# Kernel tuning notes

Measured on AMD Instinct MI355X. Metric: run time of the kernel, lower is better.

The kernel has to match this reference:

```python
import jax, jax.numpy as jnp
import numpy as np

V, H, I, L = 32000, 1024, 2048, 4
NH, NKV, HD = 16, 8, 64
E, K = 4, 2
B, S = 2, 1024
NEG = jnp.finfo(jnp.float32).min


def setup_inputs() -> dict:
    key = jax.random.key(0)
    ks = jax.random.split(key, 11)
    w = lambda k, shape: jax.random.normal(k, shape, jnp.float32) * 0.02
    return dict(
        input_ids=jax.random.randint(ks[0], (B, S), 0, V),
        embed=w(ks[1], (V, H)),
        Wq=w(ks[2], (L, H, NH * HD)),
        Wk=w(ks[3], (L, H, NKV * HD)),
        Wv=w(ks[4], (L, H, NKV * HD)),
        Wo=w(ks[5], (L, NH * HD, H)),
        ln1=jnp.ones((L, H), jnp.float32),
        ln2=jnp.ones((L, H), jnp.float32),
        gate=w(ks[6], (L, H, E)),
        Wg=w(ks[7], (L, E, H, I)),
        Wu=w(ks[8], (L, E, H, I)),
        Wd=w(ks[9], (L, E, I, H)),
        norm_w=jnp.ones((H,), jnp.float32),
        lm_head=w(ks[10], (H, V)),
    )


def rmsnorm(x, w, eps=1e-6):
    var = jnp.mean(x * x, axis=-1, keepdims=True)
    return w * (x * jax.lax.rsqrt(var + eps))


def forward(input_ids, embed, Wq, Wk, Wv, Wo, ln1, ln2, gate, Wg, Wu, Wd, norm_w, lm_head):
    b, s = input_ids.shape
    h = embed[input_ids]  # [B,S,H]
    mask = jnp.where(jnp.triu(jnp.ones((s, s), bool), 1), NEG, 0.0)[None, None]  # causal [1,1,S,S]
    inv_sqrt_hd = 1.0 / np.sqrt(HD)
    rep = NH // NKV

    def step(h, p):
        wq, wk, wv, wo, l1, l2, gw, wg, wu, wd = p
        x = rmsnorm(h, l1)
        q = (x @ wq).reshape(b, s, NH, HD).transpose(0, 2, 1, 3)    # [B,NH,S,HD]
        k = (x @ wk).reshape(b, s, NKV, HD).transpose(0, 2, 1, 3)   # [B,NKV,S,HD]
        v = (x @ wv).reshape(b, s, NKV, HD).transpose(0, 2, 1, 3)
        k = jnp.repeat(k, rep, axis=1)  # GQA repeat_kv
        v = jnp.repeat(v, rep, axis=1)
        scores = jnp.einsum('bhqd,bhkd->bhqk', q, k) * inv_sqrt_hd + mask
        attn = jax.nn.softmax(scores, axis=-1)
        o = jnp.einsum('bhqk,bhkd->bhqd', attn, v).transpose(0, 2, 1, 3).reshape(b, s, NH * HD)
        h = h + o @ wo
        # MoE FFN (top-k routing, combine via per-expert gate weights)
        x = rmsnorm(h, l2).reshape(b * s, H)              # [T,H]
        probs = jax.nn.softmax(x @ gw, axis=-1)           # [T,E]
        topk_p, topk_i = jax.lax.top_k(probs, K)          # [T,K]
        comb = jnp.sum(topk_p[..., None] * jax.nn.one_hot(topk_i, E, dtype=x.dtype), axis=1)  # [T,E]
        g = jax.nn.silu(jnp.einsum('th,ehi->eti', x, wg))  # [E,T,I]
        u = jnp.einsum('th,ehi->eti', x, wu)
        eo = jnp.einsum('eti,eih->eth', g * u, wd)         # [E,T,H]
        moe = jnp.einsum('eth,te->th', eo, comb).reshape(b, s, H)
        return h + moe, None

    h, _ = jax.lax.scan(step, h, (Wq, Wk, Wv, Wo, ln1, ln2, gate, Wg, Wu, Wd))
    return rmsnorm(h, norm_w) @ lm_head  # [B,S,V]


def reference(input_ids, embed, Wq, Wk, Wv, Wo, ln1, ln2, gate, Wg, Wu, Wd, norm_w, lm_head):
    return forward(input_ids, embed, Wq, Wk, Wv, Wo, ln1, ln2, gate, Wg, Wu, Wd, norm_w, lm_head)
```

## Files before the change

kernel.cpp:

```cpp
#include <hip/hip_runtime.h>

#define T_ 2048
#define H_ 1024
#define S_ 1024
#define V_ 32000
#define I_ 2048
#define NHD 1024
#define KVD 512

typedef unsigned short u16;
typedef unsigned int u32;
typedef __attribute__((ext_vector_type(8))) short s16x8;
typedef __attribute__((ext_vector_type(4))) float f32x4;

__device__ __forceinline__ u16 f2b(float f){ u32 x=__builtin_bit_cast(u32,f); return (u16)((x+0x7fffu+((x>>16)&1u))>>16); }
__device__ __forceinline__ float b2f(u16 u){ return __builtin_bit_cast(float,(u32)u<<16); }
__device__ __forceinline__ float wsum(float v){ for(int o=32;o;o>>=1) v+=__shfl_xor(v,o); return v; }
__device__ __forceinline__ float wmax(float v){ for(int o=32;o;o>>=1) v=fmaxf(v,__shfl_xor(v,o)); return v; }

__device__ __forceinline__ void gl16(const void* g, void* l){
  __builtin_amdgcn_global_load_lds(
      (const __attribute__((address_space(1))) unsigned int*)g,
      (__attribute__((address_space(3))) unsigned int*)l, 16, 0, 0);
}

__global__ void k_embed(const int* __restrict__ ids, const float* __restrict__ emb, float* __restrict__ h){
  int t = blockIdx.x;
  long src = (long)ids[t]*H_;
  ((float4*)(h + (long)t*H_))[threadIdx.x] = ((const float4*)(emb+src))[threadIdx.x];
}

__global__ void k_zero(int* c){ if(threadIdx.x<16) c[threadIdx.x]=0; }

__global__ void k_rms_sp(const float* __restrict__ h, const float* __restrict__ w,
                         u16* __restrict__ xhi, u16* __restrict__ xlo){
  int wid = threadIdx.x>>6, lane = threadIdx.x&63;
  int t = blockIdx.x*4 + wid;
  const float* row = h + (long)t*H_;
  float v[16]; float ss=0.f;
  #pragma unroll
  for(int j=0;j<16;j++){ v[j]=row[j*64+lane]; ss += v[j]*v[j]; }
  ss = wsum(ss);
  float rstd = rsqrtf(ss/(float)H_ + 1e-6f);
  #pragma unroll
  for(int j=0;j<16;j++){
    int idx=j*64+lane;
    float y = v[j]*rstd*w[idx];
    u16 hv = f2b(y);
    xhi[(long)t*H_+idx] = hv;
    xlo[(long)t*H_+idx] = f2b(y - b2f(hv));
  }
}

__global__ void k_router(const float* __restrict__ h, const float* __restrict__ lw,
                         const float* __restrict__ gate, float* __restrict__ comb,
                         int* __restrict__ lists, int* __restrict__ cnt, int2* __restrict__ epos,
                         u16* __restrict__ xhi, u16* __restrict__ xlo){
  int wid = threadIdx.x>>6, lane = threadIdx.x&63;
  int t = blockIdx.x*4+wid;
  const float* row = h + (long)t*H_;
  float v[16]; float ss=0.f;
  #pragma unroll
  for(int j=0;j<16;j++){ v[j]=row[j*64+lane]; ss+=v[j]*v[j]; }
  ss = wsum(ss);
  float rstd = rsqrtf(ss/(float)H_+1e-6f);
  float a0=0,a1=0,a2=0,a3=0;
  #pragma unroll
  for(int j=0;j<16;j++){
    int idx=j*64+lane;
    float y = v[j]*rstd*lw[idx];
    u16 hv = f2b(y);
    xhi[(long)t*H_+idx] = hv;
    xlo[(long)t*H_+idx] = f2b(y - b2f(hv));
    float4 g4 = ((const float4*)gate)[idx];
    a0 += y*g4.x; a1 += y*g4.y; a2 += y*g4.z; a3 += y*g4.w;
  }
  a0=wsum(a0); a1=wsum(a1); a2=wsum(a2); a3=wsum(a3);
  if(lane==0){
    float p[4]={a0,a1,a2,a3};
    float m = fmaxf(fmaxf(p[0],p[1]),fmaxf(p[2],p[3]));
    float s=0; for(int e=0;e<4;e++){ p[e]=__expf(p[e]-m); s+=p[e]; }
    for(int e=0;e<4;e++) p[e]/=s;
    int i1=0; for(int e=1;e<4;e++) if(p[e]>p[i1]) i1=e;
    int i2=-1; for(int e=0;e<4;e++){ if(e==i1) continue; if(i2<0||p[e]>p[i2]) i2=e; }
    float* c = comb + (long)t*4;
    for(int e=0;e<4;e++) c[e] = (e==i1||e==i2)? p[e] : 0.f;
    int p1 = atomicAdd(&cnt[i1],1); lists[i1*T_+p1]=t;
    int p2 = atomicAdd(&cnt[i2],1); lists[i2*T_+p2]=t;
    epos[t] = make_int2((p1<<2)|i1, (p2<<2)|i2);
  }
}

__global__ void k_transpose(const float* __restrict__ in, u16* __restrict__ hi, u16* __restrict__ lo,
                            int R, int C, long zi, long zo){
  __shared__ float tile[32][33];
  in += (long)blockIdx.z*zi; hi += (long)blockIdx.z*zo; if(lo) lo += (long)blockIdx.z*zo;
  int c0 = blockIdx.x*32, r0 = blockIdx.y*32;
  int tx = threadIdx.x, ty = threadIdx.y;
  #pragma unroll
  for(int i=0;i<4;i++) tile[ty+8*i][tx] = in[(long)(r0+ty+8*i)*C + c0+tx];
  __syncthreads();
  #pragma unroll
  for(int i=0;i<4;i++){
    int cc=ty+8*i; float v = tile[tx][cc];
    u16 hv = f2b(v);
    long idx = (long)(c0+cc)*R + r0+tx;
    hi[idx] = hv;
    if(lo) lo[idx] = f2b(v - b2f(hv));
  }
}

__global__ void k_wtrans(const float* __restrict__ Wq, const float* __restrict__ Wk,
                         const float* __restrict__ Wv, const float* __restrict__ Wo,
                         const float* __restrict__ Wg, const float* __restrict__ Wu,
                         const float* __restrict__ Wd,
                         u16* __restrict__ qkvh, u16* __restrict__ qkvl,
                         u16* __restrict__ oh, u16* __restrict__ ol,
                         u16* __restrict__ gh, u16* __restrict__ gl_,
                         u16* __restrict__ uh, u16* __restrict__ ul,
                         u16* __restrict__ dh, u16* __restrict__ dl)
{
  __shared__ float tile[32][33];
  int id = blockIdx.x;
  const float* in; u16 *hi, *lo; int R, C, bx, by;
  if(id < 1024){ in=Wq; hi=qkvh; lo=qkvl; R=1024; C=1024; bx=id&31; by=id>>5; }
  else if(id < 1536){ id-=1024; in=Wk; hi=qkvh+1048576; lo=qkvl+1048576; R=1024; C=512; bx=id&15; by=id>>4; }
  else if(id < 2048){ id-=1536; in=Wv; hi=qkvh+1572864; lo=qkvl+1572864; R=1024; C=512; bx=id&15; by=id>>4; }
  else if(id < 3072){ id-=2048; in=Wo; hi=oh; lo=ol; R=1024; C=1024; bx=id&31; by=id>>5; }
  else if(id < 11264){ id-=3072; int z=id>>11, r2=id&2047;
    in=Wg+(size_t)z*H_*I_; hi=gh+(size_t)z*I_*H_; lo=gl_+(size_t)z*I_*H_;
    R=1024; C=2048; bx=r2&63; by=r2>>6; }
  else if(id < 19456){ id-=11264; int z=id>>11, r2=id&2047;
    in=Wu+(size_t)z*H_*I_; hi=uh+(size_t)z*I_*H_; lo=ul+(size_t)z*I_*H_;
    R=1024; C=2048; bx=r2&63; by=r2>>6; }
  else { id-=19456; int z=id>>11, r2=id&2047;
    in=Wd+(size_t)z*I_*H_; hi=dh+(size_t)z*H_*I_; lo=dl+(size_t)z*H_*I_;
    R=2048; C=1024; bx=r2&31; by=r2>>5; }
  int c0=bx*32, r0=by*32, tx=threadIdx.x, ty=threadIdx.y;
  #pragma unroll
  for(int i=0;i<4;i++) tile[ty+8*i][tx] = in[(long)(r0+ty+8*i)*C + c0+tx];
  __syncthreads();
  #pragma unroll
  for(int i=0;i<4;i++){
    int cc=ty+8*i; float v = tile[tx][cc];
    u16 hv = f2b(v);
    long idx = (long)(c0+cc)*R + r0+tx;
    hi[idx] = hv;
    lo[idx] = f2b(v - b2f(hv));
  }
}

__global__ void k_combine(float* __restrict__ h, const float* __restrict__ eo,
                          const int2* __restrict__ epos, const float* __restrict__ comb){
  int t = blockIdx.x, c = threadIdx.x;
  int2 ep = epos[t];
  int e1 = ep.x&3, p1 = ep.x>>2, e2 = ep.y&3, p2 = ep.y>>2;
  float c1 = comb[t*4+e1], c2 = comb[t*4+e2];
  float4 a = ((const float4*)(eo + (long)(e1*T_+p1)*H_))[c];
  float4 b = ((const float4*)(eo + (long)(e2*T_+p2)*H_))[c];
  float4* hp = (float4*)(h + (long)t*H_) + c;
  float4 hv = *hp;
  hv.x += c1*a.x + c2*b.x; hv.y += c1*a.y + c2*b.y;
  hv.z += c1*a.z + c2*b.z; hv.w += c1*a.w + c2*b.w;
  *hp = hv;
}

__global__ __launch_bounds__(256) void k_flash(
  const u16* __restrict__ qh_g, const u16* __restrict__ ql_g,
  const u16* __restrict__ kh_g, const u16* __restrict__ kl_g,
  const u16* __restrict__ vth_g, const u16* __restrict__ vtl_g,
  u16* __restrict__ oh_g, u16* __restrict__ ol_g)
{
  __shared__ alignas(16) u16 Qh[4096], Ql[4096];
  __shared__ alignas(16) u16 KVh[8192], KVl[8192];
  __shared__ alignas(16) u16 Ph[8192], Pl[8192];
  const int qt = blockIdx.x, hh = blockIdx.y, b = blockIdx.z;
  const int hk = hh>>1;
  const int lane = threadIdx.x&63, w = threadIdx.x>>6;
  const int rA = lane&15, kg = (lane>>4)*8;

  {
    const u16* qp = qh_g + ((long)(b*1024+qt*64))*NHD + hh*64;
    const u16* qp2= ql_g + ((long)(b*1024+qt*64))*NHD + hh*64;
    #pragma unroll
    for(int s=0;s<2;s++){
      int idx=s*4+w, hf=idx>>2, g=idx&3;
      int row = g*16 + (lane>>2);
      int c8  = hf*32 + (lane&3)*8;
      gl16(qp  + (long)row*NHD + c8, &Qh[hf*2048 + g*512]);
      gl16(qp2 + (long)row*NHD + c8, &Ql[hf*2048 + g*512]);
    }
  }

  f32x4 Oa[4];
  float mrun[4], lrun[4];
  #pragma unroll
  for(int jn=0;jn<4;jn++){ f32x4 zv={0.f,0.f,0.f,0.f}; Oa[jn]=zv; }
  #pragma unroll
  for(int r=0;r<4;r++){ mrun[r]=-3.0e38f; lrun[r]=0.f; }

  const int ktend = (qt>>1)+1;
  for(int kt=0; kt<ktend; kt++){
    __syncthreads();
    {
      const u16* kp = kh_g + ((long)(b*1024+kt*128))*KVD + hk*64;
      const u16* kp2= kl_g + ((long)(b*1024+kt*128))*KVD + hk*64;
      #pragma unroll
      for(int s=0;s<4;s++){
        int idx=s*4+w, hf=idx>>3, g=idx&7;
        int row = g*16 + (lane>>2);
        int c8  = hf*32 + (lane&3)*8;
        gl16(kp  + (long)row*KVD + c8, &KVh[hf*4096 + g*512]);
        gl16(kp2 + (long)row*KVD + c8, &KVl[hf*4096 + g*512]);
      }
    }
    __syncthreads();

    f32x4 Sf[8];
    #pragma unroll
    for(int j=0;j<8;j++){ f32x4 zv={0.f,0.f,0.f,0.f}; Sf[j]=zv; }
    #pragma unroll
    for(int k2=0;k2<2;k2++){
      s16x8 ah,al,bh[8],bl[8];
      int q = w*16+rA;
      ah=*(const s16x8*)&Qh[k2*2048 + q*32 + kg];
      al=*(const s16x8*)&Ql[k2*2048 + q*32 + kg];
      #pragma unroll
      for(int j=0;j<8;j++){
        int ky = j*16+rA;
        bh[j]=*(const s16x8*)&KVh[k2*4096 + ky*32 + kg];
        bl[j]=*(const s16x8*)&KVl[k2*4096 + ky*32 + kg];
      }
      #pragma unroll
      for(int j=0;j<8;j++){
        Sf[j]=__builtin_amdgcn_mfma_f32_16x16x32_bf16(ah,bh[j],Sf[j],0,0,0);
        Sf[j]=__builtin_amdgcn_mfma_f32_16x16x32_bf16(ah,bl[j],Sf[j],0,0,0);
        Sf[j]=__builtin_amdgcn_mfma_f32_16x16x32_bf16(al,bh[j],Sf[j],0,0,0);
      }
    }

    const bool last = (kt==ktend-1);
    #pragma unroll
    for(int j=0;j<8;j++)
      #pragma unroll
      for(int r=0;r<4;r++){
        float sv = Sf[j][r]*0.125f;
        if(last){
          int qr = qt*64 + w*16 + ((lane>>4)<<2) + r;
          int ky = kt*128 + j*16 + (lane&15);
          if(ky>qr) sv = -3.0e38f;
        }
        Sf[j][r]=sv;
      }

    float mt[4];
    #pragma unroll
    for(int r=0;r<4;r++){
      float v = Sf[0][r];
      #pragma unroll
      for(int j=1;j<8;j++) v = fmaxf(v, Sf[j][r]);
      v=fmaxf(v,__shfl_xor(v,1)); v=fmaxf(v,__shfl_xor(v,2));
      v=fmaxf(v,__shfl_xor(v,4)); v=fmaxf(v,__shfl_xor(v,8));
      mt[r]=v;
    }

    #pragma unroll
    for(int r=0;r<4;r++){
      float mo=mrun[r];
      float mn=fmaxf(mo,mt[r]);
      float al_=__expf(mo-mn);
      mrun[r]=mn;
      lrun[r]*=al_;
      #pragma unroll
      for(int jn=0;jn<4;jn++) Oa[jn][r]*=al_;
    }

    float ls[4];
    #pragma unroll
    for(int r=0;r<4;r++) ls[r]=0.f;
    #pragma unroll
    for(int j=0;j<8;j++)
      #pragma unroll
      for(int r=0;r<4;r++){
        int q  = w*16+((lane>>4)<<2)+r;
        int ky = j*16+(lane&15);
        float pv=__expf(Sf[j][r]-mrun[r]);
        ls[r]+=pv;
        u16 hv=f2b(pv);
        int a=(ky>>5)*2048 + q*32 + (ky&31);
        Ph[a]=hv; Pl[a]=f2b(pv-b2f(hv));
      }
    #pragma unroll
    for(int r=0;r<4;r++){
      float v=ls[r];
      v+=__shfl_xor(v,1); v+=__shfl_xor(v,2); v+=__shfl_xor(v,4); v+=__shfl_xor(v,8);
      lrun[r]+=v;
    }
    __syncthreads();

    {
      const u16* vp = vth_g + (long)b*((long)KVD*S_) + (long)(hk*64)*S_ + kt*128;
      const u16* vp2= vtl_g + (long)b*((long)KVD*S_) + (long)(hk*64)*S_ + kt*128;
      #pragma unroll
      for(int s=0;s<4;s++){
        int idx=s*4+w, ks=idx>>2, g=idx&3;
        int dr = g*16 + (lane>>2);
        int k8 = (lane&3)*8;
        gl16(vp  + (long)dr*S_ + ks*32 + k8, &KVh[ks*2048 + g*512]);
        gl16(vp2 + (long)dr*S_ + ks*32 + k8, &KVl[ks*2048 + g*512]);
      }
    }
    __syncthreads();

    #pragma unroll
    for(int ks=0;ks<4;ks++){
      s16x8 pah,pal,vbh[4],vbl[4];
      int q = w*16+rA;
      pah=*(const s16x8*)&Ph[ks*2048 + q*32 + kg];
      pal=*(const s16x8*)&Pl[ks*2048 + q*32 + kg];
      #pragma unroll
      for(int jn=0;jn<4;jn++){
        int d = jn*16+rA;
        vbh[jn]=*(const s16x8*)&KVh[ks*2048 + d*32 + kg];
        vbl[jn]=*(const s16x8*)&KVl[ks*2048 + d*32 + kg];
      }
      #pragma unroll
      for(int jn=0;jn<4;jn++){
        Oa[jn]=__builtin_amdgcn_mfma_f32_16x16x32_bf16(pah,vbh[jn],Oa[jn],0,0,0);
        Oa[jn]=__builtin_amdgcn_mfma_f32_16x16x32_bf16(pah,vbl[jn],Oa[jn],0,0,0);
        Oa[jn]=__builtin_amdgcn_mfma_f32_16x16x32_bf16(pal,vbh[jn],Oa[jn],0,0,0);
      }
    }
  }

  #pragma unroll
  for(int jn=0;jn<4;jn++)
    #pragma unroll
    for(int r=0;r<4;r++){
      long t = (long)b*1024 + qt*64 + w*16+((lane>>4)<<2)+r;
      int col = hh*64 + jn*16 + (lane&15);
      float ov = Oa[jn][r] / lrun[r];
      u16 hv=f2b(ov);
      oh_g[t*NHD+col]=hv;
      ol_g[t*NHD+col]=f2b(ov-b2f(hv));
    }
}

__global__ __launch_bounds__(256) void k_qkv(
  const u16* __restrict__ xhi, const u16* __restrict__ xlo,
  const u16* __restrict__ Bh, const u16* __restrict__ Bl,
  u16* __restrict__ qhi, u16* __restrict__ qlo,
  u16* __restrict__ khi, u16* __restrict__ klo,
  u16* __restrict__ vthi, u16* __restrict__ vtlo)
{
  __shared__ alignas(16) u16 As[2*128*64], Bs[2*128*64];
  const int m0=blockIdx.x*128, n0=blockIdx.y*128;
  const int tid=threadIdx.x, lane=tid&63, w=tid>>6, wr=w>>1, wc=w&1;
  const int rsub = lane>>3;
  const int col8 = ((lane&7) ^ (rsub&7))*8;
  const int kq = lane>>4;
  f32x4 acc[4][4];
  #pragma unroll
  for(int i=0;i<4;i++)
    #pragma unroll
    for(int j=0;j<4;j++){ f32x4 zv={0.f,0.f,0.f,0.f}; acc[i][j]=zv; }

  for(int kt=0;kt<16;kt++){
    const int k0=kt*64;
    __syncthreads();
    #pragma unroll
    for(int s=0;s<4;s++){
      int ch=s*4+w; int row=ch*8+rsub;
      gl16(xhi + (long)(m0+row)*H_ + k0+col8, &As[ch*512]);
      gl16(xlo + (long)(m0+row)*H_ + k0+col8, &As[8192+ch*512]);
      gl16(Bh  + (long)(n0+row)*H_ + k0+col8, &Bs[ch*512]);
      gl16(Bl  + (long)(n0+row)*H_ + k0+col8, &Bs[8192+ch*512]);
    }
    __syncthreads();
    #pragma unroll
    for(int ks=0;ks<2;ks++){
      s16x8 ah[4],al[4],bh[4],bl[4];
      #pragma unroll
      for(int i=0;i<4;i++){
        int row = wr*64+i*16+(lane&15);
        int sl = ((ks*4+kq) ^ (row&7))*8;
        ah[i]=*(const s16x8*)&As[row*64+sl];
        al[i]=*(const s16x8*)&As[8192+row*64+sl];
      }
      #pragma unroll
      for(int j=0;j<4;j++){
        int row = wc*64+j*16+(lane&15);
        int sl = ((ks*4+kq) ^ (row&7))*8;
        bh[j]=*(const s16x8*)&Bs[row*64+sl];
        bl[j]=*(const s16x8*)&Bs[8192+row*64+sl];
      }
      #pragma unroll
      for(int i=0;i<4;i++)
        #pragma unroll
        for(int j=0;j<4;j++){
          acc[i][j]=__builtin_amdgcn_mfma_f32_16x16x32_bf16(ah[i],bh[j],acc[i][j],0,0,0);
          acc[i][j]=__builtin_amdgcn_mfma_f32_16x16x32_bf16(ah[i],bl[j],acc[i][j],0,0,0);
          acc[i][j]=__builtin_amdgcn_mfma_f32_16x16x32_bf16(al[i],bh[j],acc[i][j],0,0,0);
        }
    }
  }

  #pragma unroll
  for(int i=0;i<4;i++){
    #pragma unroll
    for(int j=0;j<4;j++){
      const int gm0 = m0 + wr*64 + i*16 + ((lane>>4)<<2);
      const int gn  = n0 + wc*64 + j*16 + (lane&15);
      #pragma unroll
      for(int r=0;r<4;r++){
        const int gm = gm0+r;
        float v = acc[i][j][r];
        u16 hv = f2b(v);
        u16 lv = f2b(v - b2f(hv));
        if(gn < 1024){
          long idx=(long)gm*NHD+gn; qhi[idx]=hv; qlo[idx]=lv;
        } else if(gn < 1536){
          long idx=(long)gm*KVD+(gn-1024); khi[idx]=hv; klo[idx]=lv;
        } else {
          long idx=((long)(gm>>10)<<19) + (long)(gn-1536)*S_ + (gm&1023);
          vthi[idx]=hv; vtlo[idx]=lv;
        }
      }
    }
  }
}

__global__ __launch_bounds__(256) void k_moe_ug(
  const u16* __restrict__ xhi, const u16* __restrict__ xlo,
  const u16* __restrict__ Wuh, const u16* __restrict__ Wul,
  const u16* __restrict__ Wgh, const u16* __restrict__ Wgl,
  u16* __restrict__ guh, u16* __restrict__ gul,
  const int* __restrict__ lists, const int* __restrict__ cntp)
{
  const int bb = blockIdx.x;
  const int xcd = bb&7, bidx = bb>>3;
  const int grp = xcd + 8*(bidx>>4);
  const int mslot = bidx&15;
  const int e = grp>>5;
  const int n0 = (grp&31)*64;
  const int m0 = mslot*128;
  const int ce = cntp[e];
  if(m0>=ce) return;
  const int* ridx = lists + e*T_;
  const u16* Buh_g = Wuh + (size_t)e*H_*I_;
  const u16* Bul_g = Wul + (size_t)e*H_*I_;
  const u16* Bgh_g = Wgh + (size_t)e*H_*I_;
  const u16* Bgl_g = Wgl + (size_t)e*H_*I_;
  __shared__ alignas(16) u16 Ah[128*64], Al[128*64];
  __shared__ alignas(16) u16 Buh[64*64], Bul[64*64], Bgh[64*64], Bgl[64*64];
  const int tid=threadIdx.x, lane=tid&63, w=tid>>6;
  const int wr=w>>1, wc=w&1;
  const int rsub = lane>>3;
  const int col8 = ((lane&7) ^ (rsub&7))*8;
  const int kq = lane>>4;
  int arA[4];
  #pragma unroll
  for(int s=0;s<4;s++){ int idx=m0 + (s*4+w)*8 + rsub; arA[s]=ridx[idx<ce?idx:ce-1]; }
  f32x4 au[4][2], ag[4][2];
  #pragma unroll
  for(int i=0;i<4;i++)
    #pragma unroll
    for(int j=0;j<2;j++){ f32x4 zv={0.f,0.f,0.f,0.f}; au[i][j]=zv; ag[i][j]=zv; }

  for(int kt=0;kt<16;kt++){
    const int k0=kt*64;
    __syncthreads();
    #pragma unroll
    for(int s=0;s<4;s++){
      int ch=s*4+w;
      gl16(xhi + (long)arA[s]*H_ + k0+col8, &Ah[ch*512]);
      gl16(xlo + (long)arA[s]*H_ + k0+col8, &Al[ch*512]);
    }
    #pragma unroll
    for(int s=0;s<2;s++){
      int ch=s*4+w;
      int brow = n0 + ch*8 + rsub;
      gl16(Buh_g + (long)brow*H_ + k0+col8, &Buh[ch*512]);
      gl16(Bul_g + (long)brow*H_ + k0+col8, &Bul[ch*512]);
      gl16(Bgh_g + (long)brow*H_ + k0+col8, &Bgh[ch*512]);
      gl16(Bgl_g + (long)brow*H_ + k0+col8, &Bgl[ch*512]);
    }
    __syncthreads();
    #pragma unroll
    for(int ks=0;ks<2;ks++){
      s16x8 fah[4],fal[4],fbuh[2],fbul[2],fbgh[2],fbgl[2];
      #pragma unroll
      for(int i=0;i<4;i++){
        int row = wr*64+i*16+(lane&15);
        int sl = ((ks*4+kq) ^ (row&7))*8;
        fah[i]=*(const s16x8*)&Ah[row*64+sl];
        fal[i]=*(const s16x8*)&Al[row*64+sl];
      }
      #pragma unroll
      for(int j=0;j<2;j++){
        int row = wc*32+j*16+(lane&15);
        int sl = ((ks*4+kq) ^ (row&7))*8;
        fbuh[j]=*(const s16x8*)&Buh[row*64+sl];
        fbul[j]=*(const s16x8*)&Bul[row*64+sl];
        fbgh[j]=*(const s16x8*)&Bgh[row*64+sl];
        fbgl[j]=*(const s16x8*)&Bgl[row*64+sl];
      }
      #pragma unroll
      for(int i=0;i<4;i++)
        #pragma unroll
        for(int j=0;j<2;j++){
          au[i][j]=__builtin_amdgcn_mfma_f32_16x16x32_bf16(fah[i],fbuh[j],au[i][j],0,0,0);
          au[i][j]=__builtin_amdgcn_mfma_f32_16x16x32_bf16(fah[i],fbul[j],au[i][j],0,0,0);
          au[i][j]=__builtin_amdgcn_mfma_f32_16x16x32_bf16(fal[i],fbuh[j],au[i][j],0,0,0);
          ag[i][j]=__builtin_amdgcn_mfma_f32_16x16x32_bf16(fah[i],fbgh[j],ag[i][j],0,0,0);
          ag[i][j]=__builtin_amdgcn_mfma_f32_16x16x32_bf16(fah[i],fbgl[j],ag[i][j],0,0,0);
          ag[i][j]=__builtin_amdgcn_mfma_f32_16x16x32_bf16(fal[i],fbgh[j],ag[i][j],0,0,0);
        }
    }
  }

  #pragma unroll
  for(int i=0;i<4;i++){
    #pragma unroll
    for(int j=0;j<2;j++){
      const int gm0 = m0 + wr*64 + i*16 + ((lane>>4)<<2);
      const int gn  = n0 + wc*32 + j*16 + (lane&15);
      #pragma unroll
      for(int r=0;r<4;r++){
        const int gm = gm0+r;
        if(gm<ce){
          float uu=au[i][j][r], gg=ag[i][j][r];
          float val = (gg/(1.f+__expf(-gg)))*uu;
          long idx = (long)(e*T_+gm)*I_ + gn;
          u16 hv=f2b(val);
          guh[idx]=hv; gul[idx]=f2b(val-b2f(hv));
        }
      }
    }
  }
}

template<int BM,int BN,int WM,int WN,int BKT,bool SPL,int EPI,int CM,int GATH,bool SWZ>
__launch_bounds__(WM*WN*64)
__global__ void k_gemm(const u16* __restrict__ Ahip, const u16* __restrict__ Alop,
                       const u16* __restrict__ Bhip, const u16* __restrict__ Blop,
                       void* __restrict__ Cp, void* __restrict__ auxp,
                       const int* __restrict__ cntp,
                       int Kdim, int lda, int ldb, int ldc,
                       long zA, long zB, int zBdiv, long zC,
                       float scale)
{
  constexpr int NT = WM*WN*64;
  constexpr int Wv = NT/64;
  constexpr int WMT = BM/WM, WNT = BN/WN;
  constexpr int MF = WMT/16, NF = WNT/16;
  constexpr int LPR = BKT/8;
  constexpr int LR  = 64/LPR;
  constexpr int ACn = (BM/LR)/Wv;
  constexpr int BCn = (BN/LR)/Wv;
  constexpr int KS  = BKT/32;
  static_assert(ACn>=1 && BCn>=1, "chunks");
  __shared__ alignas(16) u16 As[(SPL?2:1)*BM*BKT];
  __shared__ alignas(16) u16 Bs[(SPL?2:1)*BN*BKT];
  __shared__ float Cs[EPI==8?WM:1][EPI==8?16:1][EPI==8?(BN+4):1];
  constexpr int SL = T_/BM;
  int m0, n0, eid_ = 0, cnt = 0;
  if constexpr (GATH==3){
    eid_ = blockIdx.x/SL; m0 = (blockIdx.x%SL)*BM;
    cnt = cntp[eid_]; if(m0>=cnt) return;
    n0 = blockIdx.y*BN;
  } else if constexpr (GATH==4){
    constexpr int NTN = H_/BN;
    const int bb = blockIdx.x;
    const int xcd = bb&7, bidx = bb>>3;
    const int grp = xcd + 8*(bidx/SL);
    const int mslot = bidx%SL;
    eid_ = grp/NTN; n0 = (grp%NTN)*BN; m0 = mslot*BM;
    cnt = cntp[eid_]; if(m0>=cnt) return;
  } else if constexpr (SWZ){
    int nx = gridDim.x;
    int l = blockIdx.y*nx + blockIdx.x;
    int q = (nx*gridDim.y)>>3;
    int wid = (l&7)*q + (l>>3);
    m0 = (wid % nx)*BM; n0 = (wid / nx)*BN;
  } else {
    m0 = blockIdx.x*BM; n0 = blockIdx.y*BN;
  }
  if (CM==1 && n0 > m0) return;
  const int z = blockIdx.z;
  const int tid = threadIdx.x, lane = tid&63, w = tid>>6;
  const int wr = w/WN, wc = w%WN;
  const int rsub = lane/LPR;
  const int col8 = (((lane%LPR) ^ (rsub&(LPR-1))))*8;
  const int kq = lane>>4;
  const u16* Ahi = Ahip + (long)z*zA + (GATH>=3 ? (long)eid_*T_*lda : 0);
  const u16* Alo = SPL ? (Alop + (long)z*zA + (GATH>=3 ? (long)eid_*T_*lda : 0)) : (const u16*)nullptr;
  const u16* Bh  = Bhip + (long)(z/zBdiv)*zB + (GATH>=3 ? (long)eid_*zB : 0);
  const u16* Bl  = SPL ? (Blop + (long)(z/zBdiv)*zB + (GATH>=3 ? (long)eid_*zB : 0)) : (const u16*)nullptr;

  f32x4 acc[MF][NF];
  #pragma unroll
  for(int i=0;i<MF;i++)
    #pragma unroll
    for(int j=0;j<NF;j++){ f32x4 zv={0.f,0.f,0.f,0.f}; acc[i][j]=zv; }

  int ktend = Kdim/BKT;
  if (CM==2){ int lim=(m0+BM)/BKT; if(lim<ktend) ktend=lim; }

  for(int kt=0;kt<ktend;kt++){
    const int k0 = kt*BKT;
    __syncthreads();
    #pragma unroll
    for(int s=0;s<ACn;s++){
      int ch = s*Wv + w;
      int arow = m0 + ch*LR + rsub;
      if constexpr (GATH>=3){ arow = arow < cnt ? arow : cnt-1; }
      gl16(Ahi + (long)arow*lda + k0+col8, &As[ch*512]);
      if constexpr (SPL) gl16(Alo + (long)arow*lda + k0+col8, &As[BM*BKT + ch*512]);
    }
    #pragma unroll
    for(int s=0;s<BCn;s++){
      int ch = s*Wv + w;
      int brow = n0 + ch*LR + rsub;
      gl16(Bh + (long)brow*ldb + k0+col8, &Bs[ch*512]);
      if constexpr (SPL) gl16(Bl + (long)brow*ldb + k0+col8, &Bs[BN*BKT + ch*512]);
    }
    __syncthreads();
    #pragma unroll
    for(int ks=0;ks<KS;ks++){
      s16x8 ah[MF], al[MF], bh[NF], bl[NF];
      #pragma unroll
      for(int i=0;i<MF;i++){
        int row = wr*WMT+i*16+(lane&15);
        int sl = ((ks*4+kq) ^ (row&(LPR-1)))*8;
        ah[i]=*(const s16x8*)&As[row*BKT+sl];
        if constexpr (SPL) al[i]=*(const s16x8*)&As[BM*BKT+row*BKT+sl];
      }
      #pragma unroll
      for(int j=0;j<NF;j++){
        int row = wc*WNT+j*16+(lane&15);
        int sl = ((ks*4+kq) ^ (row&(LPR-1)))*8;
        bh[j]=*(const s16x8*)&Bs[row*BKT+sl];
        if constexpr (SPL) bl[j]=*(const s16x8*)&Bs[BN*BKT+row*BKT+sl];
      }
      #pragma unroll
      for(int i=0;i<MF;i++)
        #pragma unroll
        for(int j=0;j<NF;j++){
          acc[i][j]=__builtin_amdgcn_mfma_f32_16x16x32_bf16(ah[i],bh[j],acc[i][j],0,0,0);
          if constexpr (SPL){
            acc[i][j]=__builtin_amdgcn_mfma_f32_16x16x32_bf16(ah[i],bl[j],acc[i][j],0,0,0);
            acc[i][j]=__builtin_amdgcn_mfma_f32_16x16x32_bf16(al[i],bh[j],acc[i][j],0,0,0);
          }
        }
    }
  }

  if constexpr (EPI==8){
    float* C = (float*)Cp + (long)z*zC;
    #pragma unroll
    for(int i=0;i<MF;i++){
      __syncthreads();
      #pragma unroll
      for(int j=0;j<NF;j++)
        #pragma unroll
        for(int r=0;r<4;r++)
          Cs[wr][((lane>>4)<<2)+r][wc*WNT + j*16 + (lane&15)] = acc[i][j][r]*scale;
      __syncthreads();
      const int rrow = tid>>3;
      const int wri = rrow>>4, r16 = rrow&15;
      const long gm = m0 + wri*WMT + i*16 + r16;
      #pragma unroll
      for(int s=0;s<BN/32;s++){
        int c0 = ((tid&7) + s*8)*4;
        float4 vv = { Cs[wri][r16][c0], Cs[wri][r16][c0+1], Cs[wri][r16][c0+2], Cs[wri][r16][c0+3] };
        *(float4*)(C + gm*ldc + n0 + c0) = vv;
      }
    }
    return;
  }

  #pragma unroll
  for(int i=0;i<MF;i++){
    #pragma unroll
    for(int j=0;j<NF;j++){
      const int gm0 = m0 + wr*WMT + i*16 + ((lane>>4)<<2);
      const int gn  = n0 + wc*WNT + j*16 + (lane&15);
      #pragma unroll
      for(int r=0;r<4;r++){
        const int gm = gm0+r;
        const float v = acc[i][j][r];
        const bool live = (GATH==0) || (gm < cnt);
        if constexpr (EPI==1){
          if(live) ((float*)Cp + (long)z*zC)[(long)gm*ldc+gn] = v*scale;
        } else if constexpr (EPI==2){
          float* C = (float*)Cp; C[(long)gm*ldc+gn] += v;
        } else if constexpr (EPI==7){
          if(live) ((float*)Cp)[(long)(eid_*T_+gm)*ldc+gn] = v*scale;
        } else if constexpr (EPI==9){
          u16* Ch = (u16*)Cp + (long)z*zC;
          u16* Cl = (u16*)auxp + (long)z*zC;
          long idx = (long)gm*ldc+gn;
          u16 hv = f2b(v);
          Ch[idx]=hv; Cl[idx]=f2b(v-b2f(hv));
        }
      }
    }
  }
}

extern "C" void kernel_launch(void* const* d_in, const int* in_sizes, int n_in,
                              void* d_out, int out_size, void* d_ws, size_t ws_size,
                              hipStream_t stream)
{
  (void)in_sizes; (void)n_in; (void)out_size;
  const int*   ids   = (const int*)d_in[0];
  const float* emb   = (const float*)d_in[1];
  const float* Wq    = (const float*)d_in[2];
  const float* Wk    = (const float*)d_in[3];
  const float* Wv    = (const float*)d_in[4];
  const float* Wo    = (const float*)d_in[5];
  const float* ln1   = (const float*)d_in[6];
  const float* ln2   = (const float*)d_in[7];
  const float* gate  = (const float*)d_in[8];
  const float* Wg    = (const float*)d_in[9];
  const float* Wu    = (const float*)d_in[10];
  const float* Wd    = (const float*)d_in[11];
  const float* normw = (const float*)d_in[12];
  const float* lmh   = (const float*)d_in[13];

  char* p = (char*)d_ws;
  auto carve = [&](size_t bytes)->void*{ void* r=p; p += (bytes+255)&~(size_t)255; return r; };
  float* h    = (float*)carve((size_t)T_*H_*4);
  u16*   xhi  = (u16*)  carve((size_t)T_*H_*2);
  u16*   xlo  = (u16*)  carve((size_t)T_*H_*2);
  u16*   qhi  = (u16*)  carve((size_t)T_*NHD*2);
  u16*   qlo  = (u16*)  carve((size_t)T_*NHD*2);
  u16*   khi  = (u16*)  carve((size_t)T_*KVD*2);
  u16*   klo  = (u16*)  carve((size_t)T_*KVD*2);
  u16*   vthi = (u16*)  carve((size_t)T_*KVD*2);
  u16*   vtlo = (u16*)  carve((size_t)T_*KVD*2);
  u16*   ohi  = (u16*)  carve((size_t)T_*NHD*2);
  u16*   olo  = (u16*)  carve((size_t)T_*NHD*2);
  float* comb = (float*)carve((size_t)T_*4*4);
  int*   cnt  = (int*)  carve((size_t)16*4);
  int*   lists= (int*)  carve((size_t)4*T_*4);
  int2*  epos = (int2*) carve((size_t)T_*8);
  char*  U    = (char*) carve((size_t)112*1024*1024);
  u16*   wp   = (u16*)  carve((size_t)56623104*2);
  if ((size_t)(p - (char*)d_ws) > ws_size) return;

  u16*   guh  = (u16*)U;
  u16*   gul  = (u16*)(U + 33554432);
  float* eo   = (float*)(U + 67108864);

  u16 *WqkvTh = wp,          *WqkvTl = wp+2097152;
  u16 *WoTh = wp+4194304,    *WoTl = wp+5242880;
  u16 *WgTh = wp+6291456,    *WgTl = wp+14680064;
  u16 *WuTh = wp+23068672,   *WuTl = wp+31457280;
  u16 *WdTh = wp+39845888,   *WdTl = wp+48234496;

  dim3 tb(32,8);

  k_embed<<<T_,256,0,stream>>>(ids, emb, h);
  k_zero<<<1,64,0,stream>>>(cnt);

  for(int l=0;l<4;l++){
    k_wtrans<<<27648,tb,0,stream>>>(
      Wq+(size_t)l*H_*NHD, Wk+(size_t)l*H_*KVD, Wv+(size_t)l*H_*KVD, Wo+(size_t)l*NHD*H_,
      Wg+(size_t)l*4*H_*I_, Wu+(size_t)l*4*H_*I_, Wd+(size_t)l*4*I_*H_,
      WqkvTh, WqkvTl, WoTh, WoTl, WgTh, WgTl, WuTh, WuTl, WdTh, WdTl);

    k_rms_sp<<<T_/4,256,0,stream>>>(h, ln1+(size_t)l*H_, xhi, xlo);

    k_qkv<<<dim3(16,16),256,0,stream>>>(xhi, xlo, WqkvTh, WqkvTl, qhi, qlo, khi, klo, vthi, vtlo);

    k_flash<<<dim3(16,16,2),256,0,stream>>>(qhi, qlo, khi, klo, vthi, vtlo, ohi, olo);

    k_gemm<64,128,2,2,64,true,2,0,0,false><<<dim3(32,8,1),256,0,stream>>>(
      ohi, olo, WoTh, WoTl, h, nullptr, nullptr, NHD, NHD, NHD, H_, 0,0,1,0, 0.f);

    k_router<<<T_/4,256,0,stream>>>(h, ln2+(size_t)l*H_, gate+(size_t)l*H_*4, comb, lists, cnt+l*4, epos, xhi, xlo);

    k_moe_ug<<<2048,256,0,stream>>>(xhi, xlo, WuTh, WuTl, WgTh, WgTl, guh, gul, lists, cnt+l*4);
    k_gemm<128,128,2,2,64,true,7,0,4,false><<<512,256,0,stream>>>(
      guh, gul, WdTh, WdTl, eo, nullptr, cnt+l*4, I_, I_, I_, H_, 0, (long)I_*H_, 1, 0, 1.f);
    k_combine<<<T_,256,0,stream>>>(h, eo, epos, comb);
  }

  k_rms_sp<<<T_/4,256,0,stream>>>(h, normw, xhi, xlo);
  k_transpose<<<dim3(1000,32),tb,0,stream>>>(lmh, wp, nullptr, H_, V_, 0,0);
  k_gemm<128,128,2,2,64,false,8,0,0,true><<<dim3(16,250,1),256,0,stream>>>(
    xhi, nullptr, wp, nullptr, (float*)d_out, nullptr, nullptr, H_, H_, H_, V_, 0,0,1,0, 1.f);
}
```

Baseline: 1.894 ms.

## Restructure flash attention with larger tiles and K/V prefetch; pipeline LM-head GEMM

The flash attention kernel now processes 128 query rows per block with 512 threads. Q fragments are held in registers, and K and V get separate LDS buffers so the next K tile's load overlaps the P·V compute, with fewer barriers per iteration. The GEMM template gains an optional double-buffered LDS pipeline, enabled only for the final LM-head GEMM. Smaller changes fold the counter zeroing into the embed kernel, skip the unused low-half write in the final rmsnorm, and remove dead template paths. LDS use per block rises considerably, which can cut occupancy.

```diff
diff --git a/kernel.cpp b/kernel.cpp
--- a/kernel.cpp
+++ b/kernel.cpp
@@ -16,7 +16,6 @@
 __device__ __forceinline__ u16 f2b(float f){ u32 x=__builtin_bit_cast(u32,f); return (u16)((x+0x7fffu+((x>>16)&1u))>>16); }
 __device__ __forceinline__ float b2f(u16 u){ return __builtin_bit_cast(float,(u32)u<<16); }
 __device__ __forceinline__ float wsum(float v){ for(int o=32;o;o>>=1) v+=__shfl_xor(v,o); return v; }
-__device__ __forceinline__ float wmax(float v){ for(int o=32;o;o>>=1) v=fmaxf(v,__shfl_xor(v,o)); return v; }
 
 __device__ __forceinline__ void gl16(const void* g, void* l){
   __builtin_amdgcn_global_load_lds(
@@ -24,13 +23,13 @@
       (__attribute__((address_space(3))) unsigned int*)l, 16, 0, 0);
 }
 
-__global__ void k_embed(const int* __restrict__ ids, const float* __restrict__ emb, float* __restrict__ h){
+__global__ void k_embed(const int* __restrict__ ids, const float* __restrict__ emb,
+                        float* __restrict__ h, int* __restrict__ cnt){
+  if(blockIdx.x==0 && threadIdx.x<16) cnt[threadIdx.x]=0;
   int t = blockIdx.x;
   long src = (long)ids[t]*H_;
   ((float4*)(h + (long)t*H_))[threadIdx.x] = ((const float4*)(emb+src))[threadIdx.x];
 }
-
-__global__ void k_zero(int* c){ if(threadIdx.x<16) c[threadIdx.x]=0; }
 
 __global__ void k_rms_sp(const float* __restrict__ h, const float* __restrict__ w,
                          u16* __restrict__ xhi, u16* __restrict__ xlo){
@@ -48,7 +47,7 @@
     float y = v[j]*rstd*w[idx];
     u16 hv = f2b(y);
     xhi[(long)t*H_+idx] = hv;
-    xlo[(long)t*H_+idx] = f2b(y - b2f(hv));
+    if(xlo) xlo[(long)t*H_+idx] = f2b(y - b2f(hv));
   }
 }
 
@@ -165,30 +164,40 @@
   *hp = hv;
 }
 
-__global__ __launch_bounds__(256) void k_flash(
+__global__ __launch_bounds__(512) void k_flash(
   const u16* __restrict__ qh_g, const u16* __restrict__ ql_g,
   const u16* __restrict__ kh_g, const u16* __restrict__ kl_g,
   const u16* __restrict__ vth_g, const u16* __restrict__ vtl_g,
   u16* __restrict__ oh_g, u16* __restrict__ ol_g)
 {
-  __shared__ alignas(16) u16 Qh[4096], Ql[4096];
-  __shared__ alignas(16) u16 KVh[8192], KVl[8192];
-  __shared__ alignas(16) u16 Ph[8192], Pl[8192];
+  __shared__ alignas(16) u16 Kh[8192], Kl[8192];
+  __shared__ alignas(16) u16 Vh[8192], Vl[8192];
+  __shared__ alignas(16) u16 Ph[16384], Pl[16384];
   const int qt = blockIdx.x, hh = blockIdx.y, b = blockIdx.z;
   const int hk = hh>>1;
   const int lane = threadIdx.x&63, w = threadIdx.x>>6;
   const int rA = lane&15, kg = (lane>>4)*8;
 
+  s16x8 qfh[2], qfl[2];
   {
-    const u16* qp = qh_g + ((long)(b*1024+qt*64))*NHD + hh*64;
-    const u16* qp2= ql_g + ((long)(b*1024+qt*64))*NHD + hh*64;
+    long t = (long)(b*1024+qt*128) + w*16 + rA;
+    const u16* qp = qh_g + t*NHD + hh*64;
+    const u16* qp2= ql_g + t*NHD + hh*64;
+    qfh[0]=*(const s16x8*)(qp + kg);      qfh[1]=*(const s16x8*)(qp + 32 + kg);
+    qfl[0]=*(const s16x8*)(qp2 + kg);     qfl[1]=*(const s16x8*)(qp2 + 32 + kg);
+  }
+
+  const int ktend = qt+1;
+  {
+    const u16* kp = kh_g + ((long)(b*1024))*KVD + hk*64;
+    const u16* kp2= kl_g + ((long)(b*1024))*KVD + hk*64;
     #pragma unroll
     for(int s=0;s<2;s++){
-      int idx=s*4+w, hf=idx>>2, g=idx&3;
+      int idx=s*8+w, hf=idx>>3, g=idx&7;
       int row = g*16 + (lane>>2);
       int c8  = hf*32 + (lane&3)*8;
-      gl16(qp  + (long)row*NHD + c8, &Qh[hf*2048 + g*512]);
-      gl16(qp2 + (long)row*NHD + c8, &Ql[hf*2048 + g*512]);
+      gl16(kp  + (long)row*KVD + c8, &Kh[hf*4096 + g*512]);
+      gl16(kp2 + (long)row*KVD + c8, &Kl[hf*4096 + g*512]);
     }
   }
 
@@ -199,43 +208,39 @@
   #pragma unroll
   for(int r=0;r<4;r++){ mrun[r]=-3.0e38f; lrun[r]=0.f; }
 
-  const int ktend = (qt>>1)+1;
+  __syncthreads();
+
   for(int kt=0; kt<ktend; kt++){
-    __syncthreads();
     {
-      const u16* kp = kh_g + ((long)(b*1024+kt*128))*KVD + hk*64;
-      const u16* kp2= kl_g + ((long)(b*1024+kt*128))*KVD + hk*64;
-      #pragma unroll
-      for(int s=0;s<4;s++){
-        int idx=s*4+w, hf=idx>>3, g=idx&7;
-        int row = g*16 + (lane>>2);
-        int c8  = hf*32 + (lane&3)*8;
-        gl16(kp  + (long)row*KVD + c8, &KVh[hf*4096 + g*512]);
-        gl16(kp2 + (long)row*KVD + c8, &KVl[hf*4096 + g*512]);
-      }
-    }
-    __syncthreads();
+      const u16* vp = vth_g + (long)b*((long)KVD*S_) + (long)(hk*64)*S_ + kt*128;
+      const u16* vp2= vtl_g + (long)b*((long)KVD*S_) + (long)(hk*64)*S_ + kt*128;
+      #pragma unroll
+      for(int s=0;s<2;s++){
+        int idx=s*8+w, ks=idx>>2, g=idx&3;
+        int dr = g*16 + (lane>>2);
+        int k8 = (lane&3)*8;
+        gl16(vp  + (long)dr*S_ + ks*32 + k8, &Vh[ks*2048 + g*512]);
+        gl16(vp2 + (long)dr*S_ + ks*32 + k8, &Vl[ks*2048 + g*512]);
+      }
+    }
 
     f32x4 Sf[8];
     #pragma unroll
     for(int j=0;j<8;j++){ f32x4 zv={0.f,0.f,0.f,0.f}; Sf[j]=zv; }
     #pragma unroll
     for(int k2=0;k2<2;k2++){
-      s16x8 ah,al,bh[8],bl[8];
-      int q = w*16+rA;
-      ah=*(const s16x8*)&Qh[k2*2048 + q*32 + kg];
-      al=*(const s16x8*)&Ql[k2*2048 + q*32 + kg];
+      s16x8 bh[8],bl[8];
       #pragma unroll
       for(int j=0;j<8;j++){
         int ky = j*16+rA;
-        bh[j]=*(const s16x8*)&KVh[k2*4096 + ky*32 + kg];
-        bl[j]=*(const s16x8*)&KVl[k2*4096 + ky*32 + kg];
+        bh[j]=*(const s16x8*)&Kh[k2*4096 + ky*32 + kg];
+        bl[j]=*(const s16x8*)&Kl[k2*4096 + ky*32 + kg];
       }
       #pragma unroll
       for(int j=0;j<8;j++){
-        Sf[j]=__builtin_amdgcn_mfma_f32_16x16x32_bf16(ah,bh[j],Sf[j],0,0,0);
-        Sf[j]=__builtin_amdgcn_mfma_f32_16x16x32_bf16(ah,bl[j],Sf[j],0,0,0);
-        Sf[j]=__builtin_amdgcn_mfma_f32_16x16x32_bf16(al,bh[j],Sf[j],0,0,0);
+        Sf[j]=__builtin_amdgcn_mfma_f32_16x16x32_bf16(qfh[k2],bh[j],Sf[j],0,0,0);
+        Sf[j]=__builtin_amdgcn_mfma_f32_16x16x32_bf16(qfh[k2],bl[j],Sf[j],0,0,0);
+        Sf[j]=__builtin_amdgcn_mfma_f32_16x16x32_bf16(qfl[k2],bh[j],Sf[j],0,0,0);
       }
     }
 
@@ -246,7 +251,7 @@
       for(int r=0;r<4;r++){
         float sv = Sf[j][r]*0.125f;
         if(last){
-          int qr = qt*64 + w*16 + ((lane>>4)<<2) + r;
+          int qr = qt*128 + w*16 + ((lane>>4)<<2) + r;
           int ky = kt*128 + j*16 + (lane&15);
           if(ky>qr) sv = -3.0e38f;
         }
@@ -287,7 +292,7 @@
         float pv=__expf(Sf[j][r]-mrun[r]);
         ls[r]+=pv;
         u16 hv=f2b(pv);
-        int a=(ky>>5)*2048 + q*32 + (ky&31);
+        int a=(ky>>5)*4096 + q*32 + (ky&31);
         Ph[a]=hv; Pl[a]=f2b(pv-b2f(hv));
       }
     #pragma unroll
@@ -298,31 +303,30 @@
     }
     __syncthreads();
 
-    {
-      const u16* vp = vth_g + (long)b*((long)KVD*S_) + (long)(hk*64)*S_ + kt*128;
-      const u16* vp2= vtl_g + (long)b*((long)KVD*S_) + (long)(hk*64)*S_ + kt*128;
-      #pragma unroll
-      for(int s=0;s<4;s++){
-        int idx=s*4+w, ks=idx>>2, g=idx&3;
-        int dr = g*16 + (lane>>2);
-        int k8 = (lane&3)*8;
-        gl16(vp  + (long)dr*S_ + ks*32 + k8, &KVh[ks*2048 + g*512]);
-        gl16(vp2 + (long)dr*S_ + ks*32 + k8, &KVl[ks*2048 + g*512]);
-      }
-    }
-    __syncthreads();
+    if(kt+1<ktend){
+      const u16* kp = kh_g + ((long)(b*1024+(kt+1)*128))*KVD + hk*64;
+      const u16* kp2= kl_g + ((long)(b*1024+(kt+1)*128))*KVD + hk*64;
+      #pragma unroll
+      for(int s=0;s<2;s++){
+        int idx=s*8+w, hf=idx>>3, g=idx&7;
+        int row = g*16 + (lane>>2);
+        int c8  = hf*32 + (lane&3)*8;
+        gl16(kp  + (long)row*KVD + c8, &Kh[hf*4096 + g*512]);
+        gl16(kp2 + (long)row*KVD + c8, &Kl[hf*4096 + g*512]);
+      }
+    }
 
     #pragma unroll
     for(int ks=0;ks<4;ks++){
       s16x8 pah,pal,vbh[4],vbl[4];
       int q = w*16+rA;
-      pah=*(const s16x8*)&Ph[ks*2048 + q*32 + kg];
-      pal=*(const s16x8*)&Pl[ks*2048 + q*32 + kg];
+      pah=*(const s16x8*)&Ph[ks*4096 + q*32 + kg];
+      pal=*(const s16x8*)&Pl[ks*4096 + q*32 + kg];
       #pragma unroll
       for(int jn=0;jn<4;jn++){
         int d = jn*16+rA;
-        vbh[jn]=*(const s16x8*)&KVh[ks*2048 + d*32 + kg];
-        vbl[jn]=*(const s16x8*)&KVl[ks*2048 + d*32 + kg];
+        vbh[jn]=*(const s16x8*)&Vh[ks*2048 + d*32 + kg];
+        vbl[jn]=*(const s16x8*)&Vl[ks*2048 + d*32 + kg];
       }
       #pragma unroll
       for(int jn=0;jn<4;jn++){
@@ -331,13 +335,14 @@
         Oa[jn]=__builtin_amdgcn_mfma_f32_16x16x32_bf16(pal,vbh[jn],Oa[jn],0,0,0);
       }
     }
+    __syncthreads();
   }
 
   #pragma unroll
   for(int jn=0;jn<4;jn++)
     #pragma unroll
     for(int r=0;r<4;r++){
-      long t = (long)b*1024 + qt*64 + w*16+((lane>>4)<<2)+r;
+      long t = (long)b*1024 + qt*128 + w*16+((lane>>4)<<2)+r;
       int col = hh*64 + jn*16 + (lane&15);
       float ov = Oa[jn][r] / lrun[r];
       u16 hv=f2b(ov);
@@ -540,7 +545,7 @@
   }
 }
 
-template<int BM,int BN,int WM,int WN,int BKT,bool SPL,int EPI,int CM,int GATH,bool SWZ>
+template<int BM,int BN,int WM,int WN,int BKT,bool SPL,int EPI,int GATH,bool SWZ,bool PIPE>
 __launch_bounds__(WM*WN*64)
 __global__ void k_gemm(const u16* __restrict__ Ahip, const u16* __restrict__ Alop,
                        const u16* __restrict__ Bhip, const u16* __restrict__ Blop,
@@ -559,17 +564,15 @@
   constexpr int ACn = (BM/LR)/Wv;
   constexpr int BCn = (BN/LR)/Wv;
   constexpr int KS  = BKT/32;
+  constexpr int ABUF = (SPL?2:1)*BM*BKT;
+  constexpr int BBUF = (SPL?2:1)*BN*BKT;
   static_assert(ACn>=1 && BCn>=1, "chunks");
-  __shared__ alignas(16) u16 As[(SPL?2:1)*BM*BKT];
-  __shared__ alignas(16) u16 Bs[(SPL?2:1)*BN*BKT];
+  __shared__ alignas(16) u16 As[(PIPE?2:1)*ABUF];
+  __shared__ alignas(16) u16 Bs[(PIPE?2:1)*BBUF];
   __shared__ float Cs[EPI==8?WM:1][EPI==8?16:1][EPI==8?(BN+4):1];
   constexpr int SL = T_/BM;
   int m0, n0, eid_ = 0, cnt = 0;
-  if constexpr (GATH==3){
-    eid_ = blockIdx.x/SL; m0 = (blockIdx.x%SL)*BM;
-    cnt = cntp[eid_]; if(m0>=cnt) return;
-    n0 = blockIdx.y*BN;
-  } else if constexpr (GATH==4){
+  if constexpr (GATH==4){
     constexpr int NTN = H_/BN;
     const int bb = blockIdx.x;
     const int xcd = bb&7, bidx = bb>>3;
@@ -586,17 +589,16 @@
   } else {
     m0 = blockIdx.x*BM; n0 = blockIdx.y*BN;
   }
-  if (CM==1 && n0 > m0) return;
   const int z = blockIdx.z;
   const int tid = threadIdx.x, lane = tid&63, w = tid>>6;
   const int wr = w/WN, wc = w%WN;
   const int rsub = lane/LPR;
   const int col8 = (((lane%LPR) ^ (rsub&(LPR-1))))*8;
   const int kq = lane>>4;
-  const u16* Ahi = Ahip + (long)z*zA + (GATH>=3 ? (long)eid_*T_*lda : 0);
-  const u16* Alo = SPL ? (Alop + (long)z*zA + (GATH>=3 ? (long)eid_*T_*lda : 0)) : (const u16*)nullptr;
-  const u16* Bh  = Bhip + (long)(z/zBdiv)*zB + (GATH>=3 ? (long)eid_*zB : 0);
-  const u16* Bl  = SPL ? (Blop + (long)(z/zBdiv)*zB + (GATH>=3 ? (long)eid_*zB : 0)) : (const u16*)nullptr;
+  const u16* Ahi = Ahip + (long)z*zA + (GATH==4 ? (long)eid_*T_*lda : 0);
+  const u16* Alo = SPL ? (Alop + (long)z*zA + (GATH==4 ? (long)eid_*T_*lda : 0)) : (const u16*)nullptr;
+  const u16* Bh  = Bhip + (long)(z/zBdiv)*zB + (GATH==4 ? (long)eid_*zB : 0);
+  const u16* Bl  = SPL ? (Blop + (long)(z/zBdiv)*zB + (GATH==4 ? (long)eid_*zB : 0)) : (const u16*)nullptr;
 
   f32x4 acc[MF][NF];
   #pragma unroll
@@ -604,28 +606,28 @@
     #pragma unroll
     for(int j=0;j<NF;j++){ f32x4 zv={0.f,0.f,0.f,0.f}; acc[i][j]=zv; }
 
-  int ktend = Kdim/BKT;
-  if (CM==2){ int lim=(m0+BM)/BKT; if(lim<ktend) ktend=lim; }
-
-  for(int kt=0;kt<ktend;kt++){
+  const int ktend = Kdim/BKT;
+
+  auto stage = [&](int kt, int boA, int boB){
     const int k0 = kt*BKT;
-    __syncthreads();
     #pragma unroll
     for(int s=0;s<ACn;s++){
       int ch = s*Wv + w;
       int arow = m0 + ch*LR + rsub;
-      if constexpr (GATH>=3){ arow = arow < cnt ? arow : cnt-1; }
-      gl16(Ahi + (long)arow*lda + k0+col8, &As[ch*512]);
-      if constexpr (SPL) gl16(Alo + (long)arow*lda + k0+col8, &As[BM*BKT + ch*512]);
+      if constexpr (GATH==4){ arow = arow < cnt ? arow : cnt-1; }
+      gl16(Ahi + (long)arow*lda + k0+col8, &As[boA + ch*512]);
+      if constexpr (SPL) gl16(Alo + (long)arow*lda + k0+col8, &As[boA + BM*BKT + ch*512]);
     }
     #pragma unroll
     for(int s=0;s<BCn;s++){
       int ch = s*Wv + w;
       int brow = n0 + ch*LR + rsub;
-      gl16(Bh + (long)brow*ldb + k0+col8, &Bs[ch*512]);
-      if constexpr (SPL) gl16(Bl + (long)brow*ldb + k0+col8, &Bs[BN*BKT + ch*512]);
-    }
-    __syncthreads();
+      gl16(Bh + (long)brow*ldb + k0+col8, &Bs[boB + ch*512]);
+      if constexpr (SPL) gl16(Bl + (long)brow*ldb + k0+col8, &Bs[boB + BN*BKT + ch*512]);
+    }
+  };
+
+  auto compute = [&](int boA, int boB){
     #pragma unroll
     for(int ks=0;ks<KS;ks++){
       s16x8 ah[MF], al[MF], bh[NF], bl[NF];
@@ -633,15 +635,15 @@
       for(int i=0;i<MF;i++){
         int row = wr*WMT+i*16+(lane&15);
         int sl = ((ks*4+kq) ^ (row&(LPR-1)))*8;
-        ah[i]=*(const s16x8*)&As[row*BKT+sl];
-        if constexpr (SPL) al[i]=*(const s16x8*)&As[BM*BKT+row*BKT+sl];
+        ah[i]=*(const s16x8*)&As[boA + row*BKT+sl];
+        if constexpr (SPL) al[i]=*(const s16x8*)&As[boA + BM*BKT+row*BKT+sl];
       }
       #pragma unroll
       for(int j=0;j<NF;j++){
         int row = wc*WNT+j*16+(lane&15);
         int sl = ((ks*4+kq) ^ (row&(LPR-1)))*8;
-        bh[j]=*(const s16x8*)&Bs[row*BKT+sl];
-        if constexpr (SPL) bl[j]=*(const s16x8*)&Bs[BN*BKT+row*BKT+sl];
+        bh[j]=*(const s16x8*)&Bs[boB + row*BKT+sl];
+        if constexpr (SPL) bl[j]=*(const s16x8*)&Bs[boB + BN*BKT+row*BKT+sl];
       }
       #pragma unroll
       for(int i=0;i<MF;i++)
@@ -653,6 +655,24 @@
             acc[i][j]=__builtin_amdgcn_mfma_f32_16x16x32_bf16(al[i],bh[j],acc[i][j],0,0,0);
           }
         }
+    }
+  };
+
+  if constexpr (PIPE){
+    stage(0,0,0);
+    __syncthreads();
+    for(int kt=0;kt<ktend;kt++){
+      int cur = kt&1;
+      if(kt+1<ktend) stage(kt+1, (cur^1)*ABUF, (cur^1)*BBUF);
+      compute(cur*ABUF, cur*BBUF);
+      __syncthreads();
+    }
+  } else {
+    for(int kt=0;kt<ktend;kt++){
+      __syncthreads();
+      stage(kt,0,0);
+      __syncthreads();
+      compute(0,0);
     }
   }
 
@@ -762,8 +782,7 @@
 
   dim3 tb(32,8);
 
-  k_embed<<<T_,256,0,stream>>>(ids, emb, h);
-  k_zero<<<1,64,0,stream>>>(cnt);
+  k_embed<<<T_,256,0,stream>>>(ids, emb, h, cnt);
 
   for(int l=0;l<4;l++){
     k_wtrans<<<27648,tb,0,stream>>>(
@@ -775,21 +794,21 @@
 
     k_qkv<<<dim3(16,16),256,0,stream>>>(xhi, xlo, WqkvTh, WqkvTl, qhi, qlo, khi, klo, vthi, vtlo);
 
-    k_flash<<<dim3(16,16,2),256,0,stream>>>(qhi, qlo, khi, klo, vthi, vtlo, ohi, olo);
-
-    k_gemm<64,128,2,2,64,true,2,0,0,false><<<dim3(32,8,1),256,0,stream>>>(
+    k_flash<<<dim3(8,16,2),512,0,stream>>>(qhi, qlo, khi, klo, vthi, vtlo, ohi, olo);
+
+    k_gemm<64,128,2,2,64,true,2,0,false,false><<<dim3(32,8,1),256,0,stream>>>(
       ohi, olo, WoTh, WoTl, h, nullptr, nullptr, NHD, NHD, NHD, H_, 0,0,1,0, 0.f);
 
     k_router<<<T_/4,256,0,stream>>>(h, ln2+(size_t)l*H_, gate+(size_t)l*H_*4, comb, lists, cnt+l*4, epos, xhi, xlo);
 
     k_moe_ug<<<2048,256,0,stream>>>(xhi, xlo, WuTh, WuTl, WgTh, WgTl, guh, gul, lists, cnt+l*4);
-    k_gemm<128,128,2,2,64,true,7,0,4,false><<<512,256,0,stream>>>(
+    k_gemm<128,128,2,2,64,true,7,4,false,false><<<512,256,0,stream>>>(
       guh, gul, WdTh, WdTl, eo, nullptr, cnt+l*4, I_, I_, I_, H_, 0, (long)I_*H_, 1, 0, 1.f);
     k_combine<<<T_,256,0,stream>>>(h, eo, epos, comb);
   }
 
-  k_rms_sp<<<T_/4,256,0,stream>>>(h, normw, xhi, xlo);
+  k_rms_sp<<<T_/4,256,0,stream>>>(h, normw, xhi, nullptr);
   k_transpose<<<dim3(1000,32),tb,0,stream>>>(lmh, wp, nullptr, H_, V_, 0,0);
-  k_gemm<128,128,2,2,64,false,8,0,0,true><<<dim3(16,250,1),256,0,stream>>>(
+  k_gemm<128,128,2,2,64,false,8,0,true,true><<<dim3(16,250,1),256,0,stream>>>(
     xhi, nullptr, wp, nullptr, (float*)d_out, nullptr, nullptr, H_, H_, H_, V_, 0,0,1,0, 1.f);
 }
```

After: 2.031 ms. 7.2% more time.
